# Kernel tuning notes

Measured on AMD Instinct MI355X. Metric: run time of the kernel, lower is better.

The kernel has to match this reference:

```python
import jax, jax.numpy as jnp
import numpy as np

N, E, D = 10000, 160000, 512
H, C = 4, 128          # hidden layers: 4 heads x 128 = 512 (residual-compatible)
HF, CF = 2, 512        # final layer: 2 heads, concat=False (mean)
NEG_SLOPE = 0.2


def _gat(x, src, dst, W, a_src, a_dst, b, heads, out_c, concat):
    """PyG-style GATConv (v1 attention), no dropout (eval mode)."""
    n = x.shape[0]
    h = (x @ W).reshape(n, heads, out_c)                  # [N,H,C]
    es = (h * a_src).sum(-1)                              # [N,H]
    ed = (h * a_dst).sum(-1)                              # [N,H]
    e = jax.nn.leaky_relu(es[src] + ed[dst], NEG_SLOPE)   # [E,H]
    m = jax.ops.segment_max(e, dst, num_segments=n)       # softmax over in-edges of dst
    m = jnp.where(jnp.isfinite(m), m, 0.0)                # guard isolated nodes
    ex = jnp.exp(e - m[dst])
    den = jax.ops.segment_sum(ex, dst, num_segments=n)
    alpha = ex / (den[dst] + 1e-16)                       # [E,H]
    msg = h[src] * alpha[..., None]                       # [E,H,C]
    out = jax.ops.segment_sum(msg, dst, num_segments=n)   # [N,H,C]
    out = out.reshape(n, heads * out_c) if concat else out.mean(axis=1)
    return out + b


def setup_inputs() -> dict:
    key = jax.random.key(0)
    ks = jax.random.split(key, 16)
    s = 0.05
    return {
        "graph": jax.random.normal(ks[0], (N, D), jnp.float32),
        "edge_index": jax.random.randint(ks[1], (2, E), 0, N, dtype=jnp.int32),
        "W1": jax.random.normal(ks[2], (D, H * C), jnp.float32) * s,
        "as1": jax.random.normal(ks[3], (H, C), jnp.float32) * s,
        "ad1": jax.random.normal(ks[4], (H, C), jnp.float32) * s,
        "b1": jnp.zeros((H * C,), jnp.float32),
        "W2": jax.random.normal(ks[5], (H * C, H * C), jnp.float32) * s,
        "as2": jax.random.normal(ks[6], (H, C), jnp.float32) * s,
        "ad2": jax.random.normal(ks[7], (H, C), jnp.float32) * s,
        "b2": jnp.zeros((H * C,), jnp.float32),
        "W3": jax.random.normal(ks[8], (H * C, HF * CF), jnp.float32) * s,
        "as3": jax.random.normal(ks[9], (HF, CF), jnp.float32) * s,
        "ad3": jax.random.normal(ks[10], (HF, CF), jnp.float32) * s,
        "b3": jnp.zeros((CF,), jnp.float32),
    }


def reference(graph, edge_index, W1, as1, ad1, b1, W2, as2, ad2, b2, W3, as3, ad3, b3):
    src, dst = edge_index[0], edge_index[1]
    # layer_size=2: conv1 + convs[0] with ELU+residual, convs[1] (concat=False) residual only
    x = jax.nn.elu(_gat(graph, src, dst, W1, as1, ad1, b1, H, C, True) + graph)
    x = jax.nn.elu(_gat(x, src, dst, W2, as2, ad2, b2, H, C, True) + x)
    x = _gat(x, src, dst, W3, as3, ad3, b3, HF, CF, False) + x
    return x
```

## Files before the change

kernel.cpp:

```cpp
#include <hip/hip_runtime.h>
#include <hip/hip_bf16.h>
#include <hip/hip_fp16.h>
#include <cstddef>
#include <cstdint>


typedef _Float16 half8 __attribute__((ext_vector_type(8)));
typedef _Float16 half4v __attribute__((ext_vector_type(4)));
typedef float floatx4 __attribute__((ext_vector_type(4)));

#define AS1(p) ((const __attribute__((address_space(1))) void*)(p))
#define AS3(p) ((__attribute__((address_space(3))) void*)(p))


__global__ void count_deg(const int* __restrict__ dst, int* __restrict__ deg, int E) {
    int e = blockIdx.x * blockDim.x + threadIdx.x;
    if (e < E) atomicAdd(&deg[dst[e]], 1);
}

__global__ void scan_kernel(const int* __restrict__ deg, int* __restrict__ row_start,
                            int* __restrict__ cursor, int n) {
    __shared__ int wsum[16];
    __shared__ int carry_s;
    int tid = threadIdx.x;
    int wave = tid >> 6, lane = tid & 63;
    if (tid == 0) { carry_s = 0; row_start[0] = 0; }
    __syncthreads();
    for (int base = 0; base < n; base += 1024) {
        int i = base + tid;
        int v = (i < n) ? deg[i] : 0;
        int x = v;
#pragma unroll
        for (int off = 1; off < 64; off <<= 1) {
            int t = __shfl_up(x, off);
            if (lane >= off) x += t;
        }
        if (lane == 63) wsum[wave] = x;
        __syncthreads();
        if (wave == 0 && lane < 16) {
            int w = wsum[lane];
#pragma unroll
            for (int off = 1; off < 16; off <<= 1) {
                int t = __shfl_up(w, off);
                if (lane >= off) w += t;
            }
            wsum[lane] = w;
        }
        __syncthreads();
        int carry = carry_s;
        int incl = x + (wave ? wsum[wave - 1] : 0) + carry;
        if (i < n) { row_start[i + 1] = incl; cursor[i] = incl - v; }
        __syncthreads();
        if (tid == 1023) carry_s = incl;
        __syncthreads();
    }
}

__global__ void scatter_edges(const int* __restrict__ src, const int* __restrict__ dst,
                              int* __restrict__ cursor, int* __restrict__ srcs, int E) {
    int e = blockIdx.x * blockDim.x + threadIdx.x;
    if (e < E) {
        int p = atomicAdd(&cursor[dst[e]], 1);
        srcs[p] = src[e];
    }
}


__global__ void cast_f16(const float* __restrict__ in, _Float16* __restrict__ out, int n4) {
    int i = blockIdx.x * blockDim.x + threadIdx.x;
    if (i < n4) {
        float4 v = ((const float4*)in)[i];
        half4v o = {(_Float16)v.x, (_Float16)v.y, (_Float16)v.z, (_Float16)v.w};
        ((half4v*)out)[i] = o;
    }
}

__global__ void transpose_cast(const float* __restrict__ in, _Float16* __restrict__ out,
                               int K, int Nn) {
    __shared__ float t[32][33];
    int k0 = blockIdx.y * 32, n0 = blockIdx.x * 32;
    int tx = threadIdx.x, ty = threadIdx.y;
    for (int i = ty; i < 32; i += 8)
        t[i][tx] = in[(size_t)(k0 + i) * Nn + n0 + tx];
    __syncthreads();
    for (int i = ty; i < 32; i += 8)
        out[(size_t)(n0 + i) * K + k0 + tx] = (_Float16)t[tx][i];
}


#define BM 128
#define BN 128
#define BK 64

__global__ __launch_bounds__(256) void gemm_f16(const _Float16* __restrict__ A,
                                                const _Float16* __restrict__ Bt,
                                                _Float16* __restrict__ C,
                                                int M, int Nn, int K) {
    __shared__ _Float16 As[BM * BK];
    __shared__ _Float16 Bs[BN * BK];
    int tid = threadIdx.x;
    int lane = tid & 63, wave = tid >> 6;
    int wm = (wave & 1) * 64, wn = (wave >> 1) * 64;
    int m0 = blockIdx.y * BM, n0 = blockIdx.x * BN;
    int l15 = lane & 15, quad = lane >> 4;
    int trow = tid >> 3, tcol = tid & 7;

    floatx4 acc[4][4];
#pragma unroll
    for (int i = 0; i < 4; ++i)
#pragma unroll
        for (int j = 0; j < 4; ++j) acc[i][j] = (floatx4){0.f, 0.f, 0.f, 0.f};

    for (int k0 = 0; k0 < K; k0 += BK) {
        __syncthreads();
#pragma unroll
        for (int i = 0; i < 4; ++i) {
            int r = i * 32 + trow;
            int gr = m0 + r; if (gr >= M) gr = M - 1;
            const _Float16* gp = A + (size_t)gr * K + k0 + tcol * 8;
            _Float16* lp = As + (size_t)(i * 256 + tid) * 8;
            __builtin_amdgcn_global_load_lds(AS1(gp), AS3(lp), 16, 0, 0);
        }
#pragma unroll
        for (int i = 0; i < 4; ++i) {
            int r = i * 32 + trow;
            const _Float16* gp = Bt + (size_t)(n0 + r) * K + k0 + tcol * 8;
            _Float16* lp = Bs + (size_t)(i * 256 + tid) * 8;
            __builtin_amdgcn_global_load_lds(AS1(gp), AS3(lp), 16, 0, 0);
        }
        __syncthreads();
#pragma unroll
        for (int ks = 0; ks < BK; ks += 32) {
            half8 af[4], bfr[4];
#pragma unroll
            for (int i = 0; i < 4; ++i)
                af[i] = *(const half8*)&As[(wm + i * 16 + l15) * BK + ks + quad * 8];
#pragma unroll
            for (int j = 0; j < 4; ++j)
                bfr[j] = *(const half8*)&Bs[(wn + j * 16 + l15) * BK + ks + quad * 8];
#pragma unroll
            for (int i = 0; i < 4; ++i)
#pragma unroll
                for (int j = 0; j < 4; ++j)
                    acc[i][j] = __builtin_amdgcn_mfma_f32_16x16x32_f16(af[i], bfr[j], acc[i][j], 0, 0, 0);
        }
    }
#pragma unroll
    for (int i = 0; i < 4; ++i)
#pragma unroll
        for (int j = 0; j < 4; ++j) {
            int col = n0 + wn + j * 16 + l15;
#pragma unroll
            for (int r = 0; r < 4; ++r) {
                int row = m0 + wm + i * 16 + quad * 4 + r;
                if (row < M) C[(size_t)row * Nn + col] = (_Float16)acc[i][j][r];
            }
        }
}


__global__ void attn_coef(const _Float16* __restrict__ h, const float* __restrict__ a_src,
                          const float* __restrict__ a_dst, float* __restrict__ es,
                          float* __restrict__ ed, int NH, int Hh, int C) {
    int gw = (blockIdx.x * blockDim.x + threadIdx.x) >> 6;
    int lane = threadIdx.x & 63;
    if (gw >= NH) return;
    int hd = gw % Hh;
    const _Float16* hp = h + (size_t)gw * C;
    const float* ap = a_src + hd * C;
    const float* dp = a_dst + hd * C;
    float ss = 0.f, sd = 0.f;
    for (int c = lane; c < C; c += 64) {
        float hv = (float)hp[c];
        ss += hv * ap[c];
        sd += hv * dp[c];
    }
#pragma unroll
    for (int off = 32; off; off >>= 1) {
        ss += __shfl_down(ss, off);
        sd += __shfl_down(sd, off);
    }
    if (lane == 0) { es[gw] = ss; ed[gw] = sd; }
}


__global__ void attn_alpha(const float* __restrict__ es, const float* __restrict__ ed,
                           const int* __restrict__ row_start, const int* __restrict__ srcs,
                           float* __restrict__ alpha, int Nn, int Hh, int E) {
    int gw = (blockIdx.x * blockDim.x + threadIdx.x) >> 6;
    int lane = threadIdx.x & 63;
    if (gw >= Nn * Hh) return;
    int n = gw / Hh, hd = gw - n * Hh;
    float edn = ed[n * Hh + hd];
    int beg = row_start[n], end = row_start[n + 1];
    float m = -INFINITY;
    for (int j = beg + lane; j < end; j += 64) {
        float e = es[srcs[j] * Hh + hd] + edn;
        e = (e > 0.f) ? e : 0.2f * e;
        m = fmaxf(m, e);
    }
#pragma unroll
    for (int off = 32; off; off >>= 1) m = fmaxf(m, __shfl_xor(m, off));
    float den = 0.f;
    for (int j = beg + lane; j < end; j += 64) {
        float e = es[srcs[j] * Hh + hd] + edn;
        e = (e > 0.f) ? e : 0.2f * e;
        den += __expf(e - m);
    }
#pragma unroll
    for (int off = 32; off; off >>= 1) den += __shfl_xor(den, off);
    float inv = 1.f / (den + 1e-16f);
    for (int j = beg + lane; j < end; j += 64) {
        float e = es[srcs[j] * Hh + hd] + edn;
        e = (e > 0.f) ? e : 0.2f * e;
        alpha[(size_t)hd * E + j] = __expf(e - m) * inv;
    }
}


__global__ __launch_bounds__(256) void aggregate3_concat(
    const _Float16* __restrict__ h, const float* __restrict__ alpha,
    const int* __restrict__ row_start, const int* __restrict__ srcs,
    const float* __restrict__ bias, const float* __restrict__ x_res,
    float* __restrict__ x_out, _Float16* __restrict__ x_out_h, int E) {
    __shared__ float red[4][512];
    int n = blockIdx.x;
    int tid = threadIdx.x;
    int slot = tid >> 6, lane = tid & 63;
    int head = lane >> 4;
    int c0 = lane * 8;
    const float* al = alpha + (size_t)head * E;
    int beg = row_start[n], end = row_start[n + 1];
    float acc[8] = {};
    for (int j = beg + slot; j < end; j += 4) {
        int s = srcs[j];
        float w = al[j];
        half8 hv = *(const half8*)&h[(size_t)s * 512 + c0];
#pragma unroll
        for (int k = 0; k < 8; ++k) acc[k] += w * (float)hv[k];
    }
#pragma unroll
    for (int k = 0; k < 8; ++k) red[slot][c0 + k] = acc[k];
    __syncthreads();
    int c = tid * 2;
    size_t base = (size_t)n * 512 + c;
    float v0 = red[0][c] + red[1][c] + red[2][c] + red[3][c] + bias[c] + x_res[base];
    float v1 = red[0][c + 1] + red[1][c + 1] + red[2][c + 1] + red[3][c + 1]
               + bias[c + 1] + x_res[base + 1];
    v0 = (v0 > 0.f) ? v0 : expm1f(v0);
    v1 = (v1 > 0.f) ? v1 : expm1f(v1);
    x_out[base] = v0;
    x_out[base + 1] = v1;
    x_out_h[base] = (_Float16)v0;
    x_out_h[base + 1] = (_Float16)v1;
}

__global__ __launch_bounds__(512) void aggregate3_mean(
    const _Float16* __restrict__ h, const float* __restrict__ alpha,
    const int* __restrict__ row_start, const int* __restrict__ srcs,
    const float* __restrict__ bias, const float* __restrict__ x_res,
    float* __restrict__ out, int E) {
    __shared__ float red[4][1024];
    int n = blockIdx.x, tid = threadIdx.x;
    int slot = tid >> 7, l = tid & 127;
    int head = l >> 6;
    int c0 = l * 8;
    const float* al = alpha + (size_t)head * E;
    int beg = row_start[n], end = row_start[n + 1];
    float acc[8] = {};
    for (int j = beg + slot; j < end; j += 4) {
        int s = srcs[j];
        float w = al[j];
        half8 hv = *(const half8*)&h[(size_t)s * 1024 + c0];
#pragma unroll
        for (int k = 0; k < 8; ++k) acc[k] += w * (float)hv[k];
    }
#pragma unroll
    for (int k = 0; k < 8; ++k) red[slot][c0 + k] = acc[k];
    __syncthreads();
    if (tid < 256) {
        int c = tid * 2;
        size_t base = (size_t)n * 512 + c;
        float s0 = red[0][c] + red[1][c] + red[2][c] + red[3][c];
        float s0h = red[0][c + 512] + red[1][c + 512] + red[2][c + 512] + red[3][c + 512];
        float s1 = red[0][c + 1] + red[1][c + 1] + red[2][c + 1] + red[3][c + 1];
        float s1h = red[0][c + 513] + red[1][c + 513] + red[2][c + 513] + red[3][c + 513];
        out[base] = 0.5f * (s0 + s0h) + bias[c] + x_res[base];
        out[base + 1] = 0.5f * (s1 + s1h) + bias[c + 1] + x_res[base + 1];
    }
}


extern "C" void kernel_launch(void* const* d_in, const int* in_sizes, int n_in,
                              void* d_out, int out_size, void* d_ws, size_t ws_size,
                              hipStream_t stream) {
    const float* graph = (const float*)d_in[0];
    const int* edge_index = (const int*)d_in[1];
    const float* W1 = (const float*)d_in[2];
    const float* as1 = (const float*)d_in[3];
    const float* ad1 = (const float*)d_in[4];
    const float* b1 = (const float*)d_in[5];
    const float* W2 = (const float*)d_in[6];
    const float* as2 = (const float*)d_in[7];
    const float* ad2 = (const float*)d_in[8];
    const float* b2 = (const float*)d_in[9];
    const float* W3 = (const float*)d_in[10];
    const float* as3 = (const float*)d_in[11];
    const float* ad3 = (const float*)d_in[12];
    const float* b3 = (const float*)d_in[13];

    const int D = 512;
    int N = in_sizes[0] / D;
    int E = in_sizes[1] / 2;
    const int* src = edge_index;
    const int* dst = edge_index + E;

    char* p = (char*)d_ws;
    auto carve = [&](size_t bytes) {
        void* r = (void*)p;
        p += (bytes + 255) & ~(size_t)255;
        return r;
    };
    _Float16* Ah  = (_Float16*)carve((size_t)N * 512 * 2);
    _Float16* Wt  = (_Float16*)carve((size_t)1024 * 512 * 2);
    _Float16* h_h = (_Float16*)carve((size_t)N * 1024 * 2);
    float* x1     = (float*)carve((size_t)N * 512 * 4);
    float* x2     = (float*)carve((size_t)N * 512 * 4);
    float* es     = (float*)carve((size_t)N * 4 * 4);
    float* ed     = (float*)carve((size_t)N * 4 * 4);
    float* alpha  = (float*)carve((size_t)4 * E * 4);
    int* deg      = (int*)carve((size_t)N * 4);
    int* cur      = (int*)carve((size_t)N * 4);
    int* row_st   = (int*)carve((size_t)(N + 1) * 4);
    int* srcs     = (int*)carve((size_t)E * 4);

    hipMemsetAsync(deg, 0, (size_t)N * 4, stream);
    count_deg<<<(E + 255) / 256, 256, 0, stream>>>(dst, deg, E);
    scan_kernel<<<1, 1024, 0, stream>>>(deg, row_st, cur, N);
    scatter_edges<<<(E + 255) / 256, 256, 0, stream>>>(src, dst, cur, srcs, E);

    cast_f16<<<(N * 512 / 4 + 255) / 256, 256, 0, stream>>>(graph, Ah, N * 512 / 4);

    dim3 tblk(32, 8);
    transpose_cast<<<dim3(512 / 32, 512 / 32), tblk, 0, stream>>>(W1, Wt, 512, 512);
    gemm_f16<<<dim3(512 / BN, (N + BM - 1) / BM), 256, 0, stream>>>(Ah, Wt, h_h, N, 512, 512);
    attn_coef<<<(N * 4 + 3) / 4, 256, 0, stream>>>(h_h, as1, ad1, es, ed, N * 4, 4, 128);
    attn_alpha<<<(N * 4 + 3) / 4, 256, 0, stream>>>(es, ed, row_st, srcs, alpha, N, 4, E);
    aggregate3_concat<<<N, 256, 0, stream>>>(h_h, alpha, row_st, srcs, b1, graph, x1, Ah, E);

    transpose_cast<<<dim3(512 / 32, 512 / 32), tblk, 0, stream>>>(W2, Wt, 512, 512);
    gemm_f16<<<dim3(512 / BN, (N + BM - 1) / BM), 256, 0, stream>>>(Ah, Wt, h_h, N, 512, 512);
    attn_coef<<<(N * 4 + 3) / 4, 256, 0, stream>>>(h_h, as2, ad2, es, ed, N * 4, 4, 128);
    attn_alpha<<<(N * 4 + 3) / 4, 256, 0, stream>>>(es, ed, row_st, srcs, alpha, N, 4, E);
    aggregate3_concat<<<N, 256, 0, stream>>>(h_h, alpha, row_st, srcs, b2, x1, x2, Ah, E);

    transpose_cast<<<dim3(1024 / 32, 512 / 32), tblk, 0, stream>>>(W3, Wt, 512, 1024);
    gemm_f16<<<dim3(1024 / BN, (N + BM - 1) / BM), 256, 0, stream>>>(Ah, Wt, h_h, N, 1024, 512);
    attn_coef<<<(N * 2 + 3) / 4, 256, 0, stream>>>(h_h, as3, ad3, es, ed, N * 2, 2, 512);
    attn_alpha<<<(N * 2 + 3) / 4, 256, 0, stream>>>(es, ed, row_st, srcs, alpha, N, 2, E);
    aggregate3_mean<<<N, 512, 0, stream>>>(h_h, alpha, row_st, srcs, b3, x2, (float*)d_out, E);
}
```

Baseline: 378.3 us.

## Reorder final GAT layer to aggregate before projection and pack attention softmax

The final layer now folds the attention vectors into W3 (proj_a3) so the attention logits come straight from x. It aggregates x per head before multiplying, using a K=1024 GEMM with stacked per-head weights, and fuses the head mean, bias and residual into the GEMM epilogue. This removes the gather of 1024-wide h rows per edge in exchange for gathering 512-wide x rows with two weight sets. The attention softmax now packs several heads per wave, stores the logits and exponentials instead of recomputing them three times, and the concat aggregation unrolls by two edges. Accuracy shifts because x is gathered in fp16 and the aggregated result is rounded to fp16 before the GEMM.

```diff
diff --git a/kernel.cpp b/kernel.cpp
--- a/kernel.cpp
+++ b/kernel.cpp
@@ -75,16 +75,16 @@
     }
 }
 
-__global__ void transpose_cast(const float* __restrict__ in, _Float16* __restrict__ out,
-                               int K, int Nn) {
+__global__ void transpose_cast_g(const float* __restrict__ in, _Float16* __restrict__ out,
+                                 int R, int Cc, int in_ld, int out_ld) {
     __shared__ float t[32][33];
-    int k0 = blockIdx.y * 32, n0 = blockIdx.x * 32;
+    int r0 = blockIdx.y * 32, c0 = blockIdx.x * 32;
     int tx = threadIdx.x, ty = threadIdx.y;
     for (int i = ty; i < 32; i += 8)
-        t[i][tx] = in[(size_t)(k0 + i) * Nn + n0 + tx];
+        t[i][tx] = in[(size_t)(r0 + i) * in_ld + c0 + tx];
     __syncthreads();
     for (int i = ty; i < 32; i += 8)
-        out[(size_t)(n0 + i) * K + k0 + tx] = (_Float16)t[tx][i];
+        out[(size_t)(c0 + i) * out_ld + r0 + tx] = (_Float16)t[tx][i];
 }
 
 
@@ -158,6 +158,75 @@
         }
 }
 
+__global__ __launch_bounds__(256) void gemm_f16_ep(const _Float16* __restrict__ A,
+                                                   const _Float16* __restrict__ Bt,
+                                                   float* __restrict__ out,
+                                                   const float* __restrict__ bias,
+                                                   const float* __restrict__ xres,
+                                                   int M, int Nn, int K) {
+    __shared__ _Float16 As[BM * BK];
+    __shared__ _Float16 Bs[BN * BK];
+    int tid = threadIdx.x;
+    int lane = tid & 63, wave = tid >> 6;
+    int wm = (wave & 1) * 64, wn = (wave >> 1) * 64;
+    int m0 = blockIdx.y * BM, n0 = blockIdx.x * BN;
+    int l15 = lane & 15, quad = lane >> 4;
+    int trow = tid >> 3, tcol = tid & 7;
+
+    floatx4 acc[4][4];
+#pragma unroll
+    for (int i = 0; i < 4; ++i)
+#pragma unroll
+        for (int j = 0; j < 4; ++j) acc[i][j] = (floatx4){0.f, 0.f, 0.f, 0.f};
+
+    for (int k0 = 0; k0 < K; k0 += BK) {
+        __syncthreads();
+#pragma unroll
+        for (int i = 0; i < 4; ++i) {
+            int r = i * 32 + trow;
+            int gr = m0 + r; if (gr >= M) gr = M - 1;
+            const _Float16* gp = A + (size_t)gr * K + k0 + tcol * 8;
+            _Float16* lp = As + (size_t)(i * 256 + tid) * 8;
+            __builtin_amdgcn_global_load_lds(AS1(gp), AS3(lp), 16, 0, 0);
+        }
+#pragma unroll
+        for (int i = 0; i < 4; ++i) {
+            int r = i * 32 + trow;
+            const _Float16* gp = Bt + (size_t)(n0 + r) * K + k0 + tcol * 8;
+            _Float16* lp = Bs + (size_t)(i * 256 + tid) * 8;
+            __builtin_amdgcn_global_load_lds(AS1(gp), AS3(lp), 16, 0, 0);
+        }
+        __syncthreads();
+#pragma unroll
+        for (int ks = 0; ks < BK; ks += 32) {
+            half8 af[4], bfr[4];
+#pragma unroll
+            for (int i = 0; i < 4; ++i)
+                af[i] = *(const half8*)&As[(wm + i * 16 + l15) * BK + ks + quad * 8];
+#pragma unroll
+            for (int j = 0; j < 4; ++j)
+                bfr[j] = *(const half8*)&Bs[(wn + j * 16 + l15) * BK + ks + quad * 8];
+#pragma unroll
+            for (int i = 0; i < 4; ++i)
+#pragma unroll
+                for (int j = 0; j < 4; ++j)
+                    acc[i][j] = __builtin_amdgcn_mfma_f32_16x16x32_f16(af[i], bfr[j], acc[i][j], 0, 0, 0);
+        }
+    }
+#pragma unroll
+    for (int i = 0; i < 4; ++i)
+#pragma unroll
+        for (int j = 0; j < 4; ++j) {
+            int col = n0 + wn + j * 16 + l15;
+#pragma unroll
+            for (int r = 0; r < 4; ++r) {
+                int row = m0 + wm + i * 16 + quad * 4 + r;
+                if (row < M)
+                    out[(size_t)row * Nn + col] =
+                        0.5f * acc[i][j][r] + bias[col] + xres[(size_t)row * Nn + col];
+            }
+        }
+}
 
 __global__ void attn_coef(const _Float16* __restrict__ h, const float* __restrict__ a_src,
                           const float* __restrict__ a_dst, float* __restrict__ es,
@@ -183,37 +252,87 @@
     if (lane == 0) { es[gw] = ss; ed[gw] = sd; }
 }
 
-
-__global__ void attn_alpha(const float* __restrict__ es, const float* __restrict__ ed,
-                           const int* __restrict__ row_start, const int* __restrict__ srcs,
-                           float* __restrict__ alpha, int Nn, int Hh, int E) {
+__global__ void attn_coef_shared(const _Float16* __restrict__ x, const float* __restrict__ a_src,
+                                 const float* __restrict__ a_dst, float* __restrict__ es,
+                                 float* __restrict__ ed, int NH, int Hh, int C) {
     int gw = (blockIdx.x * blockDim.x + threadIdx.x) >> 6;
     int lane = threadIdx.x & 63;
-    if (gw >= Nn * Hh) return;
+    if (gw >= NH) return;
     int n = gw / Hh, hd = gw - n * Hh;
-    float edn = ed[n * Hh + hd];
+    const _Float16* hp = x + (size_t)n * C;
+    const float* ap = a_src + hd * C;
+    const float* dp = a_dst + hd * C;
+    float ss = 0.f, sd = 0.f;
+    for (int c = lane; c < C; c += 64) {
+        float hv = (float)hp[c];
+        ss += hv * ap[c];
+        sd += hv * dp[c];
+    }
+#pragma unroll
+    for (int off = 32; off; off >>= 1) {
+        ss += __shfl_down(ss, off);
+        sd += __shfl_down(sd, off);
+    }
+    if (lane == 0) { es[gw] = ss; ed[gw] = sd; }
+}
+
+__global__ void proj_a3(const float* __restrict__ W3, const float* __restrict__ as3,
+                        const float* __restrict__ ad3, float* __restrict__ wes,
+                        float* __restrict__ wed) {
+    int gw = (blockIdx.x * blockDim.x + threadIdx.x) >> 6;
+    int lane = threadIdx.x & 63;
+    int k = gw & 511, h = (gw >> 9) & 1, sel = gw >> 10;
+    const float* a = (sel ? ad3 : as3) + h * 512;
+    const float* row = W3 + (size_t)k * 1024 + h * 512;
+    float s = 0.f;
+    for (int c = lane; c < 512; c += 64) s += row[c] * a[c];
+#pragma unroll
+    for (int off = 32; off; off >>= 1) s += __shfl_down(s, off);
+    if (lane == 0) (sel ? wed : wes)[h * 512 + k] = s;
+}
+
+
+template <int H>
+__global__ __launch_bounds__(256) void attn_alpha_packed(
+    const float* __restrict__ es, const float* __restrict__ ed,
+    const int* __restrict__ row_start, const int* __restrict__ srcs,
+    float* __restrict__ alpha, int Nn, int E) {
+    const int EP = 64 / H;
+    int wave = threadIdx.x >> 6, lane = threadIdx.x & 63;
+    int n = blockIdx.x * 4 + wave;
+    if (n >= Nn) return;
+    int h = lane & (H - 1);
+    int eslot = lane / H;
+    float edn = ed[n * H + h];
     int beg = row_start[n], end = row_start[n + 1];
     float m = -INFINITY;
-    for (int j = beg + lane; j < end; j += 64) {
-        float e = es[srcs[j] * Hh + hd] + edn;
-        e = (e > 0.f) ? e : 0.2f * e;
+    for (int j0 = beg; j0 < end; j0 += EP) {
+        int j = j0 + eslot;
+        float e = -INFINITY;
+        if (j < end) {
+            e = es[srcs[j] * H + h] + edn;
+            e = (e > 0.f) ? e : 0.2f * e;
+            alpha[(size_t)h * E + j] = e;
+        }
         m = fmaxf(m, e);
     }
 #pragma unroll
-    for (int off = 32; off; off >>= 1) m = fmaxf(m, __shfl_xor(m, off));
+    for (int off = H; off < 64; off <<= 1) m = fmaxf(m, __shfl_xor(m, off));
     float den = 0.f;
-    for (int j = beg + lane; j < end; j += 64) {
-        float e = es[srcs[j] * Hh + hd] + edn;
-        e = (e > 0.f) ? e : 0.2f * e;
-        den += __expf(e - m);
-    }
-#pragma unroll
-    for (int off = 32; off; off >>= 1) den += __shfl_xor(den, off);
+    for (int j0 = beg; j0 < end; j0 += EP) {
+        int j = j0 + eslot;
+        if (j < end) {
+            float w = __expf(alpha[(size_t)h * E + j] - m);
+            alpha[(size_t)h * E + j] = w;
+            den += w;
+        }
+    }
+#pragma unroll
+    for (int off = H; off < 64; off <<= 1) den += __shfl_xor(den, off);
     float inv = 1.f / (den + 1e-16f);
-    for (int j = beg + lane; j < end; j += 64) {
-        float e = es[srcs[j] * Hh + hd] + edn;
-        e = (e > 0.f) ? e : 0.2f * e;
-        alpha[(size_t)hd * E + j] = __expf(e - m) * inv;
+    for (int j0 = beg; j0 < end; j0 += EP) {
+        int j = j0 + eslot;
+        if (j < end) alpha[(size_t)h * E + j] *= inv;
     }
 }
 
@@ -232,7 +351,18 @@
     const float* al = alpha + (size_t)head * E;
     int beg = row_start[n], end = row_start[n + 1];
     float acc[8] = {};
-    for (int j = beg + slot; j < end; j += 4) {
+    int j = beg + slot;
+    for (; j + 4 < end; j += 8) {
+        int s0 = srcs[j], s1 = srcs[j + 4];
+        float w0 = al[j], w1 = al[j + 4];
+        half8 h0 = *(const half8*)&h[(size_t)s0 * 512 + c0];
+        half8 h1 = *(const half8*)&h[(size_t)s1 * 512 + c0];
+#pragma unroll
+        for (int k = 0; k < 8; ++k) acc[k] += w0 * (float)h0[k];
+#pragma unroll
+        for (int k = 0; k < 8; ++k) acc[k] += w1 * (float)h1[k];
+    }
+    if (j < end) {
         int s = srcs[j];
         float w = al[j];
         half8 hv = *(const half8*)&h[(size_t)s * 512 + c0];
@@ -255,39 +385,63 @@
     x_out_h[base + 1] = (_Float16)v1;
 }
 
-__global__ __launch_bounds__(512) void aggregate3_mean(
-    const _Float16* __restrict__ h, const float* __restrict__ alpha,
+
+__global__ __launch_bounds__(256) void aggregate_x_dual(
+    const _Float16* __restrict__ x, const float* __restrict__ alpha,
     const int* __restrict__ row_start, const int* __restrict__ srcs,
-    const float* __restrict__ bias, const float* __restrict__ x_res,
-    float* __restrict__ out, int E) {
+    _Float16* __restrict__ y, int E) {
     __shared__ float red[4][1024];
-    int n = blockIdx.x, tid = threadIdx.x;
-    int slot = tid >> 7, l = tid & 127;
-    int head = l >> 6;
-    int c0 = l * 8;
-    const float* al = alpha + (size_t)head * E;
+    int n = blockIdx.x;
+    int tid = threadIdx.x;
+    int slot = tid >> 6, lane = tid & 63;
+    int c0 = lane * 8;
+    const float* al0 = alpha;
+    const float* al1 = alpha + E;
     int beg = row_start[n], end = row_start[n + 1];
-    float acc[8] = {};
-    for (int j = beg + slot; j < end; j += 4) {
+    float a0[8] = {}, a1[8] = {};
+    int j = beg + slot;
+    for (; j + 4 < end; j += 8) {
+        int s0 = srcs[j], s1 = srcs[j + 4];
+        float u0 = al0[j], v0 = al1[j];
+        float u1 = al0[j + 4], v1 = al1[j + 4];
+        half8 h0 = *(const half8*)&x[(size_t)s0 * 512 + c0];
+        half8 h1 = *(const half8*)&x[(size_t)s1 * 512 + c0];
+#pragma unroll
+        for (int k = 0; k < 8; ++k) {
+            float f = (float)h0[k];
+            a0[k] += u0 * f;
+            a1[k] += v0 * f;
+        }
+#pragma unroll
+        for (int k = 0; k < 8; ++k) {
+            float f = (float)h1[k];
+            a0[k] += u1 * f;
+            a1[k] += v1 * f;
+        }
+    }
+    if (j < end) {
         int s = srcs[j];
-        float w = al[j];
-        half8 hv = *(const half8*)&h[(size_t)s * 1024 + c0];
-#pragma unroll
-        for (int k = 0; k < 8; ++k) acc[k] += w * (float)hv[k];
-    }
-#pragma unroll
-    for (int k = 0; k < 8; ++k) red[slot][c0 + k] = acc[k];
+        float u = al0[j], v = al1[j];
+        half8 hv = *(const half8*)&x[(size_t)s * 512 + c0];
+#pragma unroll
+        for (int k = 0; k < 8; ++k) {
+            float f = (float)hv[k];
+            a0[k] += u * f;
+            a1[k] += v * f;
+        }
+    }
+#pragma unroll
+    for (int k = 0; k < 8; ++k) {
+        red[slot][c0 + k] = a0[k];
+        red[slot][512 + c0 + k] = a1[k];
+    }
     __syncthreads();
-    if (tid < 256) {
-        int c = tid * 2;
-        size_t base = (size_t)n * 512 + c;
-        float s0 = red[0][c] + red[1][c] + red[2][c] + red[3][c];
-        float s0h = red[0][c + 512] + red[1][c + 512] + red[2][c + 512] + red[3][c + 512];
-        float s1 = red[0][c + 1] + red[1][c + 1] + red[2][c + 1] + red[3][c + 1];
-        float s1h = red[0][c + 513] + red[1][c + 513] + red[2][c + 513] + red[3][c + 513];
-        out[base] = 0.5f * (s0 + s0h) + bias[c] + x_res[base];
-        out[base + 1] = 0.5f * (s1 + s1h) + bias[c + 1] + x_res[base + 1];
-    }
+    int c = tid * 4;
+    half4v o;
+#pragma unroll
+    for (int k = 0; k < 4; ++k)
+        o[k] = (_Float16)(red[0][c + k] + red[1][c + k] + red[2][c + k] + red[3][c + k]);
+    *(half4v*)&y[(size_t)n * 1024 + c] = o;
 }
 
 
@@ -322,13 +476,16 @@
         return r;
     };
     _Float16* Ah  = (_Float16*)carve((size_t)N * 512 * 2);
-    _Float16* Wt  = (_Float16*)carve((size_t)1024 * 512 * 2);
+    _Float16* Wt  = (_Float16*)carve((size_t)512 * 512 * 2);
+    _Float16* Bt3 = (_Float16*)carve((size_t)512 * 1024 * 2);
     _Float16* h_h = (_Float16*)carve((size_t)N * 1024 * 2);
     float* x1     = (float*)carve((size_t)N * 512 * 4);
     float* x2     = (float*)carve((size_t)N * 512 * 4);
     float* es     = (float*)carve((size_t)N * 4 * 4);
     float* ed     = (float*)carve((size_t)N * 4 * 4);
     float* alpha  = (float*)carve((size_t)4 * E * 4);
+    float* wes3   = (float*)carve((size_t)2 * 512 * 4);
+    float* wed3   = (float*)carve((size_t)2 * 512 * 4);
     int* deg      = (int*)carve((size_t)N * 4);
     int* cur      = (int*)carve((size_t)N * 4);
     int* row_st   = (int*)carve((size_t)(N + 1) * 4);
@@ -342,21 +499,25 @@
     cast_f16<<<(N * 512 / 4 + 255) / 256, 256, 0, stream>>>(graph, Ah, N * 512 / 4);
 
     dim3 tblk(32, 8);
-    transpose_cast<<<dim3(512 / 32, 512 / 32), tblk, 0, stream>>>(W1, Wt, 512, 512);
+    int nblk4 = (N + 3) / 4;
+    transpose_cast_g<<<dim3(16, 16), tblk, 0, stream>>>(W1, Wt, 512, 512, 512, 512);
     gemm_f16<<<dim3(512 / BN, (N + BM - 1) / BM), 256, 0, stream>>>(Ah, Wt, h_h, N, 512, 512);
     attn_coef<<<(N * 4 + 3) / 4, 256, 0, stream>>>(h_h, as1, ad1, es, ed, N * 4, 4, 128);
-    attn_alpha<<<(N * 4 + 3) / 4, 256, 0, stream>>>(es, ed, row_st, srcs, alpha, N, 4, E);
+    attn_alpha_packed<4><<<nblk4, 256, 0, stream>>>(es, ed, row_st, srcs, alpha, N, E);
     aggregate3_concat<<<N, 256, 0, stream>>>(h_h, alpha, row_st, srcs, b1, graph, x1, Ah, E);
 
-    transpose_cast<<<dim3(512 / 32, 512 / 32), tblk, 0, stream>>>(W2, Wt, 512, 512);
+    transpose_cast_g<<<dim3(16, 16), tblk, 0, stream>>>(W2, Wt, 512, 512, 512, 512);
     gemm_f16<<<dim3(512 / BN, (N + BM - 1) / BM), 256, 0, stream>>>(Ah, Wt, h_h, N, 512, 512);
     attn_coef<<<(N * 4 + 3) / 4, 256, 0, stream>>>(h_h, as2, ad2, es, ed, N * 4, 4, 128);
-    attn_alpha<<<(N * 4 + 3) / 4, 256, 0, stream>>>(es, ed, row_st, srcs, alpha, N, 4, E);
+    attn_alpha_packed<4><<<nblk4, 256, 0, stream>>>(es, ed, row_st, srcs, alpha, N, E);
     aggregate3_concat<<<N, 256, 0, stream>>>(h_h, alpha, row_st, srcs, b2, x1, x2, Ah, E);
 
-    transpose_cast<<<dim3(1024 / 32, 512 / 32), tblk, 0, stream>>>(W3, Wt, 512, 1024);
-    gemm_f16<<<dim3(1024 / BN, (N + BM - 1) / BM), 256, 0, stream>>>(Ah, Wt, h_h, N, 1024, 512);
-    attn_coef<<<(N * 2 + 3) / 4, 256, 0, stream>>>(h_h, as3, ad3, es, ed, N * 2, 2, 512);
-    attn_alpha<<<(N * 2 + 3) / 4, 256, 0, stream>>>(es, ed, row_st, srcs, alpha, N, 2, E);
-    aggregate3_mean<<<N, 512, 0, stream>>>(h_h, alpha, row_st, srcs, b3, x2, (float*)d_out, E);
-}
+    transpose_cast_g<<<dim3(16, 16), tblk, 0, stream>>>(W3, Bt3, 512, 512, 1024, 1024);
+    transpose_cast_g<<<dim3(16, 16), tblk, 0, stream>>>(W3 + 512, Bt3 + 512, 512, 512, 1024, 1024);
+    proj_a3<<<512, 256, 0, stream>>>(W3, as3, ad3, wes3, wed3);
+    attn_coef_shared<<<(N * 2 + 3) / 4, 256, 0, stream>>>(Ah, wes3, wed3, es, ed, N * 2, 2, 512);
+    attn_alpha_packed<2><<<nblk4, 256, 0, stream>>>(es, ed, row_st, srcs, alpha, N, E);
+    aggregate_x_dual<<<N, 256, 0, stream>>>(Ah, alpha, row_st, srcs, h_h, E);
+    gemm_f16_ep<<<dim3(512 / BN, (N + BM - 1) / BM), 256, 0, stream>>>(
+        h_h, Bt3, (float*)d_out, b3, x2, N, 512, 1024);
+}
```

New measurement: 355.7 us. -6.0%, faster.
